# Optimization experiments

Measured on AMD Instinct MI355X. Metric: run time of the kernel, lower is better.

The kernel has to match this reference:

```python
import math
import jax, jax.numpy as jnp
import numpy as np

B, T, D, FF, E = 32, 1024, 512, 2048, 8
CAPACITY_FACTOR = 1.25
CAP = int(math.ceil(CAPACITY_FACTOR * B * T / E))  # per-expert capacity (5120)


def setup_inputs() -> dict:
    key = jax.random.key(0)
    ks = jax.random.split(key, 18)
    s = 0.02
    inp = {
        "x": jax.random.normal(ks[0], (B, T, D), dtype=jnp.float32),
        # routers (linear heads, std=0.02, zero bias)
        "Wr_sp": jax.random.normal(ks[1], (D, E)) * s,
        "br_sp": jnp.zeros((E,), jnp.float32),
        "Wr_fq": jax.random.normal(ks[2], (D, E)) * s,
        "br_fq": jnp.zeros((E,), jnp.float32),
        # shared dense FFN
        "Ws1": jax.random.normal(ks[3], (D, FF)) * s,
        "bs1": jnp.zeros((FF,), jnp.float32),
        "Ws2": jax.random.normal(ks[4], (FF, D)) * s,
        "bs2": jnp.zeros((D,), jnp.float32),
        # spatial specialist bank (E experts)
        "W1_sp": jax.random.normal(ks[5], (E, D, FF)) * s,
        "b1_sp": jnp.zeros((E, FF), jnp.float32),
        "W2_sp": jax.random.normal(ks[6], (E, FF, D)) * s,
        "b2_sp": jnp.zeros((E, D), jnp.float32),
        # spectral specialist bank (E experts)
        "W1_fq": jax.random.normal(ks[7], (E, D, FF)) * s,
        "b1_fq": jnp.zeros((E, FF), jnp.float32),
        "W2_fq": jax.random.normal(ks[8], (E, FF, D)) * s,
        "b2_fq": jnp.zeros((E, D), jnp.float32),
    }
    return inp


def _bank_residual(x2, Wr, br, W1, b1, W2, b2):
    """Top-1 capacity-routed expert bank residual. x2: [N, D]."""
    N, d = x2.shape
    e = Wr.shape[1]
    logits = x2 @ Wr + br                                  # [N, E]
    probs = jax.nn.softmax(logits, axis=-1)
    expert = jnp.argmax(probs, axis=-1)                    # [N] top-1
    gate = jnp.take_along_axis(probs, expert[:, None], axis=-1)[:, 0]
    oneh = jax.nn.one_hot(expert, e, dtype=x2.dtype)       # [N, E]
    # position of each token within its expert's queue (0-based)
    pos = (jnp.cumsum(oneh, axis=0) * oneh).sum(-1).astype(jnp.int32) - 1
    keep = pos < CAP                                       # fallback-to-shared when saturated
    slot = expert.astype(jnp.int32) * CAP + jnp.minimum(pos, CAP - 1)
    xd = jnp.where(keep[:, None], x2, 0.0)
    buf = jnp.zeros((e * CAP, d), x2.dtype).at[slot].add(xd)  # dispatch (dropped tokens add 0)
    buf = buf.reshape(e, CAP, d)
    h = jax.nn.gelu(jnp.einsum('ecd,edf->ecf', buf, W1) + b1[:, None, :], approximate=False)
    out = jnp.einsum('ecf,efd->ecd', h, W2) + b2[:, None, :]
    y = out.reshape(e * CAP, d)[slot]                      # combine (gather back)
    return y * (gate * keep.astype(x2.dtype))[:, None]


def reference(x, Wr_sp, br_sp, Wr_fq, br_fq, Ws1, bs1, Ws2, bs2,
              W1_sp, b1_sp, W2_sp, b2_sp, W1_fq, b1_fq, W2_fq, b2_fq):
    b, t, d = x.shape
    x2 = x.reshape(b * t, d)
    shared = jax.nn.gelu(x2 @ Ws1 + bs1, approximate=False) @ Ws2 + bs2
    y = shared
    y = y + _bank_residual(x2, Wr_sp, br_sp, W1_sp, b1_sp, W2_sp, b2_sp)
    y = y + _bank_residual(x2, Wr_fq, br_fq, W1_fq, b1_fq, W2_fq, b2_fq)
    return y.reshape(b, t, d)
```

## Files before the change

kernel.cpp:

```cpp
#include <hip/hip_runtime.h>
#include <hip/hip_bf16.h>
#include <math.h>

#define N_TOK 32768
#define DIMD  512
#define FFD   2048
#define NE    8
#define CAPQ  5120
#define TPE2  20
#define NBLK  128

typedef __attribute__((ext_vector_type(8))) short          bf16x8;
typedef __attribute__((ext_vector_type(4))) float          f32x4;
typedef __attribute__((ext_vector_type(8))) unsigned short u16x8;

__device__ __forceinline__ unsigned short f2bf(float f) {
  union { float f; unsigned u; } v; v.f = f;
  unsigned r = v.u + 0x7fffu + ((v.u >> 16) & 1u);
  return (unsigned short)(r >> 16);
}

__device__ __forceinline__ float gelu_f(float v) {
  float t = v * v;
  float q = fmaf(-0.0713548162f, t, -1.5957691216f);
  float w = v * q;
  float d = 1.0f + __expf(w);
  return v * __builtin_amdgcn_rcpf(d);
}

#define GLL16(gsrc, ldst)                                                      \
  __builtin_amdgcn_global_load_lds(                                            \
      (const __attribute__((address_space(1))) void*)(gsrc),                   \
      (__attribute__((address_space(3))) void*)(ldst), 16, 0, 0)

__global__ __launch_bounds__(256) void transpose_cvt3_kernel(
    const float* __restrict__ s0, const float* __restrict__ s1,
    const float* __restrict__ s2,
    unsigned short* __restrict__ d0, unsigned short* __restrict__ d1,
    unsigned short* __restrict__ d2, int R, int C) {
  __shared__ unsigned short tile[32][33];
  const int z = blockIdx.z;
  const float* in; unsigned short* out;
  if (z == 0)      { in = s0;                            out = d0; }
  else if (z <= 8) { in = s1 + (size_t)(z - 1) * R * C;  out = d1 + (size_t)(z - 1) * R * C; }
  else             { in = s2 + (size_t)(z - 9) * R * C;  out = d2 + (size_t)(z - 9) * R * C; }
  int c0 = blockIdx.x * 32, r0 = blockIdx.y * 32;
  int tx = threadIdx.x & 31, ty = threadIdx.x >> 5;
  #pragma unroll
  for (int i = 0; i < 4; i++) {
    int r = ty + i * 8;
    tile[r][tx] = f2bf(in[(size_t)(r0 + r) * C + c0 + tx]);
  }
  __syncthreads();
  #pragma unroll
  for (int i = 0; i < 4; i++) {
    int c = ty + i * 8;
    out[(size_t)(c0 + c) * R + r0 + tx] = tile[tx][c];
  }
}

__global__ __launch_bounds__(256) void router_kernel(
    const float* __restrict__ x, unsigned short* __restrict__ xb,
    const float* __restrict__ WrS, const float* __restrict__ brS,
    const float* __restrict__ WrF, const float* __restrict__ brF,
    int* __restrict__ expS, float* __restrict__ gateS,
    int* __restrict__ expF, float* __restrict__ gateF) {
  __shared__ float wS[DIMD * NE], wF[DIMD * NE];
  for (int i = threadIdx.x; i < DIMD * NE / 4; i += 256) {
    ((float4*)wS)[i] = ((const float4*)WrS)[i];
    ((float4*)wF)[i] = ((const float4*)WrF)[i];
  }
  __syncthreads();
  const int w = threadIdx.x >> 6, lane = threadIdx.x & 63;
  const int n0 = (blockIdx.x * 4 + w) * 8;
  for (int t = 0; t < 8; t++) {
    const int n = n0 + t;
    const float* xr = x + (size_t)n * DIMD + lane * 8;
    float4 xa = *(const float4*)xr, xb4 = *(const float4*)(xr + 4);
    float xv[8] = {xa.x, xa.y, xa.z, xa.w, xb4.x, xb4.y, xb4.z, xb4.w};
    u16x8 xo;
    #pragma unroll
    for (int j = 0; j < 8; j++) xo[j] = f2bf(xv[j]);
    *(u16x8*)(xb + (size_t)n * DIMD + lane * 8) = xo;
    float aS[NE], aF[NE];
    #pragma unroll
    for (int e = 0; e < NE; e++) { aS[e] = 0.f; aF[e] = 0.f; }
    #pragma unroll
    for (int j = 0; j < 8; j++) {
      const int k = lane * 8 + j;
      const float* ps = &wS[k * NE];
      const float* pf = &wF[k * NE];
      #pragma unroll
      for (int e = 0; e < NE; e++) { aS[e] += xv[j] * ps[e]; aF[e] += xv[j] * pf[e]; }
    }
    #pragma unroll
    for (int e = 0; e < NE; e++)
      for (int off = 32; off; off >>= 1) {
        aS[e] += __shfl_xor(aS[e], off);
        aF[e] += __shfl_xor(aF[e], off);
      }
    if (lane == 0) {
      float l[NE];
      #pragma unroll
      for (int e = 0; e < NE; e++) l[e] = aS[e] + brS[e];
      float m = l[0]; int am = 0;
      #pragma unroll
      for (int e = 1; e < NE; e++) if (l[e] > m) { m = l[e]; am = e; }
      float s = 0.f;
      #pragma unroll
      for (int e = 0; e < NE; e++) s += __expf(l[e] - m);
      expS[n] = am; gateS[n] = __builtin_amdgcn_rcpf(s);
      #pragma unroll
      for (int e = 0; e < NE; e++) l[e] = aF[e] + brF[e];
      m = l[0]; am = 0;
      #pragma unroll
      for (int e = 1; e < NE; e++) if (l[e] > m) { m = l[e]; am = e; }
      s = 0.f;
      #pragma unroll
      for (int e = 0; e < NE; e++) s += __expf(l[e] - m);
      expF[n] = am; gateF[n] = __builtin_amdgcn_rcpf(s);
    }
  }
}

__global__ __launch_bounds__(256) void scan_count_kernel(
    const int* __restrict__ expS, const int* __restrict__ expF,
    int* __restrict__ blockcnt) {
  const int b = blockIdx.x, t = threadIdx.x;
  const int w = t >> 6, lane = t & 63;
  const int eS_ = expS[b * 256 + t], eF_ = expF[b * 256 + t];
  __shared__ int cnt[2][4][NE];
  #pragma unroll
  for (int q = 0; q < NE; q++) {
    unsigned long long mS = __ballot(eS_ == q);
    unsigned long long mF = __ballot(eF_ == q);
    if (lane == 0) { cnt[0][w][q] = __popcll(mS); cnt[1][w][q] = __popcll(mF); }
  }
  __syncthreads();
  if (t < 16) {
    const int bank = t >> 3, q = t & 7;
    blockcnt[bank * NBLK * NE + b * NE + q] =
        cnt[bank][0][q] + cnt[bank][1][q] + cnt[bank][2][q] + cnt[bank][3][q];
  }
}

__global__ __launch_bounds__(64) void scan_base_kernel(
    const int* __restrict__ blockcnt, int* __restrict__ blockbase,
    int* __restrict__ meta) {
  __shared__ int tot[2][NE];
  const int t = threadIdx.x;
  if (t < 16) {
    const int bank = t >> 3, q = t & 7;
    int run = 0;
    for (int i = 0; i < NBLK; i++) {
      int v = blockcnt[bank * NBLK * NE + i * NE + q];
      blockbase[bank * NBLK * NE + i * NE + q] = run;
      run += v;
    }
    tot[bank][q] = run;
  }
  __syncthreads();
  if (t == 0) {
    int hb_ = 0;
    for (int q = 0; q < NE; q++) {
      int cc = tot[0][q]; if (cc > CAPQ) cc = CAPQ;
      meta[q] = cc; meta[NE + q] = hb_;
      hb_ += ((cc + 255) >> 8) << 8;
    }
    hb_ = 0;
    for (int q = 0; q < NE; q++) {
      int cc = tot[1][q]; if (cc > CAPQ) cc = CAPQ;
      meta[2 * NE + q] = cc; meta[3 * NE + q] = hb_;
      hb_ += ((cc + 255) >> 8) << 8;
    }
  }
}

__global__ __launch_bounds__(256) void scan_write_kernel(
    const int* __restrict__ expS, const int* __restrict__ expF,
    const int* __restrict__ blockbase,
    int* __restrict__ idxS, int* __restrict__ idxF) {
  const int b = blockIdx.x, t = threadIdx.x;
  const int w = t >> 6, lane = t & 63;
  const int n = b * 256 + t;
  const int eS_ = expS[n], eF_ = expF[n];
  __shared__ int wcnt[2][4][NE];
  const unsigned long long ltmask = ((unsigned long long)1 << lane) - 1;
  int rS = 0, rF = 0;
  #pragma unroll
  for (int q = 0; q < NE; q++) {
    unsigned long long mS = __ballot(eS_ == q);
    unsigned long long mF = __ballot(eF_ == q);
    if (eS_ == q) rS = __popcll(mS & ltmask);
    if (eF_ == q) rF = __popcll(mF & ltmask);
    if (lane == 0) { wcnt[0][w][q] = __popcll(mS); wcnt[1][w][q] = __popcll(mF); }
  }
  __syncthreads();
  int pS = blockbase[0 * NBLK * NE + b * NE + eS_] + rS;
  int pF = blockbase[1 * NBLK * NE + b * NE + eF_] + rF;
  #pragma unroll
  for (int wv = 0; wv < 4; wv++) {
    if (wv < w) { pS += wcnt[0][wv][eS_]; pF += wcnt[1][wv][eF_]; }
  }
  if (pS < CAPQ) idxS[eS_ * CAPQ + pS] = n;
  if (pF < CAPQ) idxF[eF_ * CAPQ + pF] = n;
}

template <int EPI, bool GATHER, bool BANKED>
__global__ __launch_bounds__(1024, 4) void gemm_kernel(
    const unsigned short* __restrict__ A,
    const unsigned short* __restrict__ Bt,
    const float* __restrict__ bias,
    const int* __restrict__ idx, const int* __restrict__ cnt,
    const int* __restrict__ hb, const float* __restrict__ gate,
    unsigned short* __restrict__ hidOut, float* __restrict__ fOut) {
  constexpr int K  = (EPI == 0) ? DIMD : FFD;
  constexpr int NC = (EPI == 0) ? FFD : DIMD;
  constexpr int NT = K / 64;

  __shared__ __align__(16) unsigned short lA[2][256 * 64];
  __shared__ __align__(16) unsigned short lB[2][256 * 64];

  const int tid = threadIdx.x;
  const int w = tid >> 6, lane = tid & 63;

  const int gx = gridDim.x;
  const int nwg = gx * gridDim.y;
  int flat = blockIdx.y * gx + blockIdx.x;
  {
    const int q8 = nwg >> 3, r8 = nwg & 7;
    const int xcd = flat & 7, loc = flat >> 3;
    flat = (xcd < r8 ? xcd * (q8 + 1) : r8 * (q8 + 1) + (xcd - r8) * q8) + loc;
  }
  const int bx = flat % gx, by = flat / gx;

  int e = 0, r0, cnte = 0;
  if (BANKED) {
    e = by / TPE2;
    r0 = (by - e * TPE2) * 256;
    cnte = cnt[e];
    if (r0 >= cnte) return;
  } else {
    r0 = by * 256;
  }

  const int srow = lane >> 3;
  const int sch  = (lane & 7) ^ srow;
  const unsigned short* aP[2];
  const unsigned short* bP[2];
  const size_t bcol0 = (size_t)(BANKED ? e * NC : 0) + (size_t)bx * 256;
  #pragma unroll
  for (int i = 0; i < 2; i++) {
    const int ri = (i * 16 + w) * 8 + srow;
    size_t arow;
    if (GATHER) {
      int s = r0 + ri;
      int tok = (s < cnte) ? idx[e * CAPQ + s] : 0;
      arow = (size_t)tok;
    } else if (BANKED) {
      arow = (size_t)(hb[e] + r0 + ri);
    } else {
      arow = (size_t)(r0 + ri);
    }
    aP[i] = A + arow * K + sch * 8;
    bP[i] = Bt + (bcol0 + ri) * K + sch * 8;
  }

  f32x4 acc[4][4];
  #pragma unroll
  for (int m = 0; m < 4; m++)
    #pragma unroll
    for (int n = 0; n < 4; n++) acc[m][n] = (f32x4){0.f, 0.f, 0.f, 0.f};

  const int wr = w >> 2, wc = w & 3;
  const int grp = lane >> 4, l15 = lane & 15;
  const int swz = l15 & 7;
  int aoff[4], boff[4], kche[2];
  #pragma unroll
  for (int m = 0; m < 4; m++) aoff[m] = (wr * 64 + m * 16 + l15) * 64;
  #pragma unroll
  for (int n = 0; n < 4; n++) boff[n] = (wc * 64 + n * 16 + l15) * 64;
  #pragma unroll
  for (int kk = 0; kk < 2; kk++) kche[kk] = ((kk * 4 + grp) ^ swz) * 8;

  auto stage = [&](int buf, int k0) {
    char* la = (char*)&lA[buf][0] + (unsigned)w * 1024;
    char* lb = (char*)&lB[buf][0] + (unsigned)w * 1024;
    #pragma unroll
    for (int i = 0; i < 2; i++) {
      GLL16(aP[i] + k0, la + i * 16384);
      GLL16(bP[i] + k0, lb + i * 16384);
    }
  };

  stage(0, 0);
  int cur = 0;
  #pragma unroll 1
  for (int t = 0; t < NT; t++) {
    if (t + 1 < NT) {
      stage(cur ^ 1, (t + 1) * 64);
      asm volatile("s_waitcnt vmcnt(4)" ::: "memory");
    } else {
      asm volatile("s_waitcnt vmcnt(0)" ::: "memory");
    }
    __builtin_amdgcn_s_barrier();
    __builtin_amdgcn_sched_barrier(0);
    const unsigned short* A_ = &lA[cur][0];
    const unsigned short* B_ = &lB[cur][0];
    #pragma unroll
    for (int kk = 0; kk < 2; kk++) {
      const int co = kche[kk];
      bf16x8 af[4], bfv[4];
      #pragma unroll
      for (int m = 0; m < 4; m++) af[m] = *(const bf16x8*)&A_[aoff[m] + co];
      #pragma unroll
      for (int n = 0; n < 4; n++) bfv[n] = *(const bf16x8*)&B_[boff[n] + co];
      __builtin_amdgcn_s_setprio(1);
      #pragma unroll
      for (int m = 0; m < 4; m++)
        #pragma unroll
        for (int n = 0; n < 4; n++)
          acc[m][n] = __builtin_amdgcn_mfma_f32_16x16x32_bf16(af[m], bfv[n], acc[m][n], 0, 0, 0);
      __builtin_amdgcn_s_setprio(0);
    }
    __builtin_amdgcn_sched_barrier(0);
    __builtin_amdgcn_s_barrier();
    cur ^= 1;
  }

  const int grp4 = grp * 4;
  if constexpr (EPI == 0) {
    const size_t hrow0 = (size_t)((BANKED ? hb[e] : 0) + r0);
    const float* bP2 = bias + (BANKED ? e * NC : 0) + bx * 256;
    #pragma unroll
    for (int m = 0; m < 4; m++)
      #pragma unroll
      for (int j = 0; j < 4; j++) {
        const int rloc = wr * 64 + m * 16 + grp4 + j;
        unsigned short* hrow = hidOut + (hrow0 + rloc) * FFD + bx * 256;
        #pragma unroll
        for (int n = 0; n < 4; n++) {
          const int cloc = wc * 64 + n * 16 + l15;
          float v = acc[m][n][j] + bP2[cloc];
          hrow[cloc] = f2bf(gelu_f(v));
        }
      }
  } else if constexpr (EPI == 1) {
    const float* bP2 = bias + bx * 256;
    #pragma unroll
    for (int m = 0; m < 4; m++)
      #pragma unroll
      for (int j = 0; j < 4; j++) {
        const int rloc = wr * 64 + m * 16 + grp4 + j;
        float* orow = fOut + (size_t)(r0 + rloc) * DIMD + bx * 256;
        #pragma unroll
        for (int n = 0; n < 4; n++) {
          const int cloc = wc * 64 + n * 16 + l15;
          orow[cloc] = acc[m][n][j] + bP2[cloc];
        }
      }
  } else {
    const float* bP2 = bias + e * NC + bx * 256;
    const int* idxe = idx + e * CAPQ + r0;
    #pragma unroll
    for (int m = 0; m < 4; m++)
      #pragma unroll
      for (int j = 0; j < 4; j++) {
        const int rloc = wr * 64 + m * 16 + grp4 + j;
        if (r0 + rloc < cnte) {
          const int tok = idxe[rloc];
          const float gv = gate[tok];
          float* orow = fOut + (size_t)tok * DIMD + bx * 256;
          #pragma unroll
          for (int n = 0; n < 4; n++) {
            const int cloc = wc * 64 + n * 16 + l15;
            orow[cloc] += (acc[m][n][j] + bP2[cloc]) * gv;
          }
        }
      }
  }
}

extern "C" void kernel_launch(void* const* d_in, const int* in_sizes, int n_in,
                              void* d_out, int out_size, void* d_ws, size_t ws_size,
                              hipStream_t stream) {
  const float* x   = (const float*)d_in[0];
  const float* WrS = (const float*)d_in[1];
  const float* brS = (const float*)d_in[2];
  const float* WrF = (const float*)d_in[3];
  const float* brF = (const float*)d_in[4];
  const float* Ws1 = (const float*)d_in[5];
  const float* bs1 = (const float*)d_in[6];
  const float* Ws2 = (const float*)d_in[7];
  const float* bs2 = (const float*)d_in[8];
  const float* W1s = (const float*)d_in[9];
  const float* b1s = (const float*)d_in[10];
  const float* W2s = (const float*)d_in[11];
  const float* b2s = (const float*)d_in[12];
  const float* W1f = (const float*)d_in[13];
  const float* b1f = (const float*)d_in[14];
  const float* W2f = (const float*)d_in[15];
  const float* b2f = (const float*)d_in[16];
  float* out = (float*)d_out;

  char* ws = (char*)d_ws;
  size_t off = 0;
  auto alloc = [&](size_t b) { char* p = ws + off; off += (b + 255) & ~(size_t)255; return p; };
  unsigned short* xb     = (unsigned short*)alloc((size_t)N_TOK * DIMD * 2);
  unsigned short* ws1t   = (unsigned short*)alloc((size_t)FFD * DIMD * 2);
  unsigned short* ws2t   = (unsigned short*)alloc((size_t)DIMD * FFD * 2);
  unsigned short* w1st   = (unsigned short*)alloc((size_t)NE * FFD * DIMD * 2);
  unsigned short* w2st   = (unsigned short*)alloc((size_t)NE * DIMD * FFD * 2);
  unsigned short* w1ft   = (unsigned short*)alloc((size_t)NE * FFD * DIMD * 2);
  unsigned short* w2ft   = (unsigned short*)alloc((size_t)NE * DIMD * FFD * 2);
  unsigned short* hidden = (unsigned short*)alloc((size_t)(N_TOK + NE * 256) * FFD * 2);
  int*   expS = (int*)alloc((size_t)N_TOK * 4);
  int*   expF = (int*)alloc((size_t)N_TOK * 4);
  float* gS   = (float*)alloc((size_t)N_TOK * 4);
  float* gF   = (float*)alloc((size_t)N_TOK * 4);
  int*   idxS = (int*)alloc((size_t)NE * CAPQ * 4);
  int*   idxF = (int*)alloc((size_t)NE * CAPQ * 4);
  int*   meta = (int*)alloc(4 * NE * 4);
  int*   blockcnt  = (int*)alloc((size_t)2 * NBLK * NE * 4);
  int*   blockbase = (int*)alloc((size_t)2 * NBLK * NE * 4);
  if (off > ws_size) return;

  int* cntS = meta;           int* hbS = meta + NE;
  int* cntF = meta + 2 * NE;  int* hbF = meta + 3 * NE;

  transpose_cvt3_kernel<<<dim3(FFD / 32, DIMD / 32, 17), 256, 0, stream>>>(
      Ws1, W1s, W1f, ws1t, w1st, w1ft, DIMD, FFD);
  transpose_cvt3_kernel<<<dim3(DIMD / 32, FFD / 32, 17), 256, 0, stream>>>(
      Ws2, W2s, W2f, ws2t, w2st, w2ft, FFD, DIMD);
  router_kernel<<<N_TOK / 32, 256, 0, stream>>>(x, xb, WrS, brS, WrF, brF, expS, gS, expF, gF);
  scan_count_kernel<<<NBLK, 256, 0, stream>>>(expS, expF, blockcnt);
  scan_base_kernel<<<1, 64, 0, stream>>>(blockcnt, blockbase, meta);
  scan_write_kernel<<<NBLK, 256, 0, stream>>>(expS, expF, blockbase, idxS, idxF);

  gemm_kernel<0, false, false><<<dim3(FFD / 256, N_TOK / 256), 1024, 0, stream>>>(
      xb, ws1t, bs1, nullptr, nullptr, nullptr, nullptr, hidden, nullptr);
  gemm_kernel<1, false, false><<<dim3(DIMD / 256, N_TOK / 256), 1024, 0, stream>>>(
      hidden, ws2t, bs2, nullptr, nullptr, nullptr, nullptr, nullptr, out);
  gemm_kernel<0, true, true><<<dim3(FFD / 256, NE * TPE2), 1024, 0, stream>>>(
      xb, w1st, b1s, idxS, cntS, hbS, nullptr, hidden, nullptr);
  gemm_kernel<2, false, true><<<dim3(DIMD / 256, NE * TPE2), 1024, 0, stream>>>(
      hidden, w2st, b2s, idxS, cntS, hbS, gS, nullptr, out);
  gemm_kernel<0, true, true><<<dim3(FFD / 256, NE * TPE2), 1024, 0, stream>>>(
      xb, w1ft, b1f, idxF, cntF, hbF, nullptr, hidden, nullptr);
  gemm_kernel<2, false, true><<<dim3(DIMD / 256, NE * TPE2), 1024, 0, stream>>>(
      hidden, w2ft, b2f, idxF, cntF, hbF, gF, nullptr, out);
}
```

Baseline: 849.0 us.

## Restructure GEMM to 512 threads with 4-stage K=32 LDS pipeline

```diff
diff --git a/kernel.cpp b/kernel.cpp
--- a/kernel.cpp
+++ b/kernel.cpp
@@ -1,6 +1,7 @@
 #include <hip/hip_runtime.h>
 #include <hip/hip_bf16.h>
 #include <math.h>
+#include <type_traits>
 
 #define N_TOK 32768
 #define DIMD  512
@@ -207,7 +208,7 @@
 }
 
 template <int EPI, bool GATHER, bool BANKED>
-__global__ __launch_bounds__(1024, 4) void gemm_kernel(
+__global__ __launch_bounds__(512, 2) void gemm_kernel(
     const unsigned short* __restrict__ A,
     const unsigned short* __restrict__ Bt,
     const float* __restrict__ bias,
@@ -216,10 +217,10 @@
     unsigned short* __restrict__ hidOut, float* __restrict__ fOut) {
   constexpr int K  = (EPI == 0) ? DIMD : FFD;
   constexpr int NC = (EPI == 0) ? FFD : DIMD;
-  constexpr int NT = K / 64;
-
-  __shared__ __align__(16) unsigned short lA[2][256 * 64];
-  __shared__ __align__(16) unsigned short lB[2][256 * 64];
+  constexpr int NT = K / 32;
+
+  __shared__ __align__(16) unsigned short sA[4][256 * 32];
+  __shared__ __align__(16) unsigned short sB[4][256 * 32];
 
   const int tid = threadIdx.x;
   const int w = tid >> 6, lane = tid & 63;
@@ -244,99 +245,120 @@
     r0 = by * 256;
   }
 
-  const int srow = lane >> 3;
-  const int sch  = (lane & 7) ^ srow;
-  const unsigned short* aP[2];
-  const unsigned short* bP[2];
+  const int srow0 = tid >> 2;
+  const int gch = (tid & 3) ^ ((tid >> 3) & 3);
+  const unsigned short* aS[2];
+  const unsigned short* bS[2];
   const size_t bcol0 = (size_t)(BANKED ? e * NC : 0) + (size_t)bx * 256;
   #pragma unroll
   for (int i = 0; i < 2; i++) {
-    const int ri = (i * 16 + w) * 8 + srow;
+    const int r = i * 128 + srow0;
     size_t arow;
     if (GATHER) {
-      int s = r0 + ri;
+      int s = r0 + r;
       int tok = (s < cnte) ? idx[e * CAPQ + s] : 0;
       arow = (size_t)tok;
     } else if (BANKED) {
-      arow = (size_t)(hb[e] + r0 + ri);
+      arow = (size_t)(hb[e] + r0 + r);
     } else {
-      arow = (size_t)(r0 + ri);
-    }
-    aP[i] = A + arow * K + sch * 8;
-    bP[i] = Bt + (bcol0 + ri) * K + sch * 8;
-  }
-
-  f32x4 acc[4][4];
-  #pragma unroll
-  for (int m = 0; m < 4; m++)
-    #pragma unroll
-    for (int n = 0; n < 4; n++) acc[m][n] = (f32x4){0.f, 0.f, 0.f, 0.f};
+      arow = (size_t)(r0 + r);
+    }
+    aS[i] = A + arow * K + gch * 8;
+    bS[i] = Bt + (bcol0 + r) * K + gch * 8;
+  }
 
   const int wr = w >> 2, wc = w & 3;
   const int grp = lane >> 4, l15 = lane & 15;
-  const int swz = l15 & 7;
-  int aoff[4], boff[4], kche[2];
-  #pragma unroll
-  for (int m = 0; m < 4; m++) aoff[m] = (wr * 64 + m * 16 + l15) * 64;
-  #pragma unroll
-  for (int n = 0; n < 4; n++) boff[n] = (wc * 64 + n * 16 + l15) * 64;
-  #pragma unroll
-  for (int kk = 0; kk < 2; kk++) kche[kk] = ((kk * 4 + grp) ^ swz) * 8;
-
-  auto stage = [&](int buf, int k0) {
-    char* la = (char*)&lA[buf][0] + (unsigned)w * 1024;
-    char* lb = (char*)&lB[buf][0] + (unsigned)w * 1024;
-    #pragma unroll
-    for (int i = 0; i < 2; i++) {
-      GLL16(aP[i] + k0, la + i * 16384);
-      GLL16(bP[i] + k0, lb + i * 16384);
-    }
+  const int kch = grp ^ ((l15 >> 1) & 3);
+  const int aBase = (wr * 128 + l15) * 32 + kch * 8;
+  const int bBase = (wc * 64 + l15) * 32 + kch * 8;
+
+  f32x4 acc[8][4];
+  #pragma unroll
+  for (int m = 0; m < 8; m++)
+    #pragma unroll
+    for (int n = 0; n < 4; n++) acc[m][n] = (f32x4){0.f, 0.f, 0.f, 0.f};
+
+  bf16x8 af[4], bfr[4];
+
+  auto stageA = [&](int sbuf, int kt) {
+    char* d = (char*)&sA[sbuf][0] + (unsigned)w * 1024;
+    const int off = kt * 32;
+    GLL16(aS[0] + off, d);
+    GLL16(aS[1] + off, d + 8192);
   };
-
-  stage(0, 0);
-  int cur = 0;
-  #pragma unroll 1
-  for (int t = 0; t < NT; t++) {
-    if (t + 1 < NT) {
-      stage(cur ^ 1, (t + 1) * 64);
-      asm volatile("s_waitcnt vmcnt(4)" ::: "memory");
-    } else {
-      asm volatile("s_waitcnt vmcnt(0)" ::: "memory");
-    }
+  auto stageB = [&](int sbuf, int kt) {
+    char* d = (char*)&sB[sbuf][0] + (unsigned)w * 1024;
+    const int off = kt * 32;
+    GLL16(bS[0] + off, d);
+    GLL16(bS[1] + off, d + 8192);
+  };
+
+  auto tile = [&](int bi, int sbuf, int kt3, auto STG, auto VM) {
+    const unsigned short* A_ = &sA[bi][0];
+    const unsigned short* B_ = &sB[bi][0];
+    #pragma unroll
+    for (int mi = 0; mi < 4; mi++) af[mi] = *(const bf16x8*)&A_[aBase + mi * 512];
+    #pragma unroll
+    for (int n = 0; n < 4; n++) bfr[n] = *(const bf16x8*)&B_[bBase + n * 512];
+    if constexpr (decltype(STG)::value) stageA(sbuf, kt3);
     __builtin_amdgcn_s_barrier();
+    asm volatile("s_waitcnt lgkmcnt(0)" ::: "memory");
     __builtin_amdgcn_sched_barrier(0);
-    const unsigned short* A_ = &lA[cur][0];
-    const unsigned short* B_ = &lB[cur][0];
-    #pragma unroll
-    for (int kk = 0; kk < 2; kk++) {
-      const int co = kche[kk];
-      bf16x8 af[4], bfv[4];
-      #pragma unroll
-      for (int m = 0; m < 4; m++) af[m] = *(const bf16x8*)&A_[aoff[m] + co];
-      #pragma unroll
-      for (int n = 0; n < 4; n++) bfv[n] = *(const bf16x8*)&B_[boff[n] + co];
-      __builtin_amdgcn_s_setprio(1);
-      #pragma unroll
-      for (int m = 0; m < 4; m++)
-        #pragma unroll
-        for (int n = 0; n < 4; n++)
-          acc[m][n] = __builtin_amdgcn_mfma_f32_16x16x32_bf16(af[m], bfv[n], acc[m][n], 0, 0, 0);
-      __builtin_amdgcn_s_setprio(0);
-    }
+    __builtin_amdgcn_s_setprio(1);
+    #pragma unroll
+    for (int mi = 0; mi < 4; mi++)
+      #pragma unroll
+      for (int n = 0; n < 4; n++)
+        acc[mi][n] = __builtin_amdgcn_mfma_f32_16x16x32_bf16(af[mi], bfr[n], acc[mi][n], 0, 0, 0);
+    __builtin_amdgcn_s_setprio(0);
     __builtin_amdgcn_sched_barrier(0);
     __builtin_amdgcn_s_barrier();
-    cur ^= 1;
-  }
+    #pragma unroll
+    for (int mi = 0; mi < 4; mi++) af[mi] = *(const bf16x8*)&A_[aBase + (4 + mi) * 512];
+    if constexpr (decltype(STG)::value) stageB(sbuf, kt3);
+    if constexpr (decltype(VM)::value == 8)
+      asm volatile("s_waitcnt vmcnt(8)" ::: "memory");
+    else if constexpr (decltype(VM)::value == 4)
+      asm volatile("s_waitcnt vmcnt(4)" ::: "memory");
+    else if constexpr (decltype(VM)::value == 0)
+      asm volatile("s_waitcnt vmcnt(0)" ::: "memory");
+    __builtin_amdgcn_s_barrier();
+    asm volatile("s_waitcnt lgkmcnt(0)" ::: "memory");
+    __builtin_amdgcn_sched_barrier(0);
+    __builtin_amdgcn_s_setprio(1);
+    #pragma unroll
+    for (int mi = 0; mi < 4; mi++)
+      #pragma unroll
+      for (int n = 0; n < 4; n++)
+        acc[4 + mi][n] = __builtin_amdgcn_mfma_f32_16x16x32_bf16(af[mi], bfr[n], acc[4 + mi][n], 0, 0, 0);
+    __builtin_amdgcn_s_setprio(0);
+    __builtin_amdgcn_sched_barrier(0);
+    __builtin_amdgcn_s_barrier();
+  };
+
+  stageA(0, 0); stageB(0, 0);
+  stageA(1, 1); stageB(1, 1);
+  stageA(2, 2); stageB(2, 2);
+  asm volatile("s_waitcnt vmcnt(8)" ::: "memory");
+  __builtin_amdgcn_s_barrier();
+
+  #pragma unroll 1
+  for (int t = 0; t < NT - 3; ++t)
+    tile(t & 3, (t + 3) & 3, t + 3, std::true_type{}, std::integral_constant<int, 8>{});
+  tile((NT - 3) & 3, 0, 0, std::false_type{}, std::integral_constant<int, 4>{});
+  tile((NT - 2) & 3, 0, 0, std::false_type{}, std::integral_constant<int, 0>{});
+  tile((NT - 1) & 3, 0, 0, std::false_type{}, std::integral_constant<int, -1>{});
 
   const int grp4 = grp * 4;
   if constexpr (EPI == 0) {
     const size_t hrow0 = (size_t)((BANKED ? hb[e] : 0) + r0);
     const float* bP2 = bias + (BANKED ? e * NC : 0) + bx * 256;
     #pragma unroll
-    for (int m = 0; m < 4; m++)
+    for (int m = 0; m < 8; m++)
       #pragma unroll
       for (int j = 0; j < 4; j++) {
-        const int rloc = wr * 64 + m * 16 + grp4 + j;
+        const int rloc = wr * 128 + m * 16 + grp4 + j;
         unsigned short* hrow = hidOut + (hrow0 + rloc) * FFD + bx * 256;
         #pragma unroll
         for (int n = 0; n < 4; n++) {
@@ -348,10 +370,10 @@
   } else if constexpr (EPI == 1) {
     const float* bP2 = bias + bx * 256;
     #pragma unroll
-    for (int m = 0; m < 4; m++)
+    for (int m = 0; m < 8; m++)
       #pragma unroll
       for (int j = 0; j < 4; j++) {
-        const int rloc = wr * 64 + m * 16 + grp4 + j;
+        const int rloc = wr * 128 + m * 16 + grp4 + j;
         float* orow = fOut + (size_t)(r0 + rloc) * DIMD + bx * 256;
         #pragma unroll
         for (int n = 0; n < 4; n++) {
@@ -363,10 +385,10 @@
     const float* bP2 = bias + e * NC + bx * 256;
     const int* idxe = idx + e * CAPQ + r0;
     #pragma unroll
-    for (int m = 0; m < 4; m++)
+    for (int m = 0; m < 8; m++)
       #pragma unroll
       for (int j = 0; j < 4; j++) {
-        const int rloc = wr * 64 + m * 16 + grp4 + j;
+        const int rloc = wr * 128 + m * 16 + grp4 + j;
         if (r0 + rloc < cnte) {
           const int tok = idxe[rloc];
           const float gv = gate[tok];
@@ -437,16 +459,16 @@
   scan_base_kernel<<<1, 64, 0, stream>>>(blockcnt, blockbase, meta);
   scan_write_kernel<<<NBLK, 256, 0, stream>>>(expS, expF, blockbase, idxS, idxF);
 
-  gemm_kernel<0, false, false><<<dim3(FFD / 256, N_TOK / 256), 1024, 0, stream>>>(
+  gemm_kernel<0, false, false><<<dim3(FFD / 256, N_TOK / 256), 512, 0, stream>>>(
       xb, ws1t, bs1, nullptr, nullptr, nullptr, nullptr, hidden, nullptr);
-  gemm_kernel<1, false, false><<<dim3(DIMD / 256, N_TOK / 256), 1024, 0, stream>>>(
+  gemm_kernel<1, false, false><<<dim3(DIMD / 256, N_TOK / 256), 512, 0, stream>>>(
       hidden, ws2t, bs2, nullptr, nullptr, nullptr, nullptr, nullptr, out);
-  gemm_kernel<0, true, true><<<dim3(FFD / 256, NE * TPE2), 1024, 0, stream>>>(
+  gemm_kernel<0, true, true><<<dim3(FFD / 256, NE * TPE2), 512, 0, stream>>>(
       xb, w1st, b1s, idxS, cntS, hbS, nullptr, hidden, nullptr);
-  gemm_kernel<2, false, true><<<dim3(DIMD / 256, NE * TPE2), 1024, 0, stream>>>(
+  gemm_kernel<2, false, true><<<dim3(DIMD / 256, NE * TPE2), 512, 0, stream>>>(
       hidden, w2st, b2s, idxS, cntS, hbS, gS, nullptr, out);
-  gemm_kernel<0, true, true><<<dim3(FFD / 256, NE * TPE2), 1024, 0, stream>>>(
+  gemm_kernel<0, true, true><<<dim3(FFD / 256, NE * TPE2), 512, 0, stream>>>(
       xb, w1ft, b1f, idxF, cntF, hbF, nullptr, hidden, nullptr);
-  gemm_kernel<2, false, true><<<dim3(DIMD / 256, NE * TPE2), 1024, 0, stream>>>(
+  gemm_kernel<2, false, true><<<dim3(DIMD / 256, NE * TPE2), 512, 0, stream>>>(
       hidden, w2ft, b2f, idxF, cntF, hbF, gF, nullptr, out);
 }
```

New measurement: 1.005 ms. 1.18x slower.
